# Performance work log

Measured on AMD Instinct MI355X. Metric: run time of the kernel, lower is better.

## Reference

```python
import jax, jax.numpy as jnp
import numpy as np

NEG_SLOPE = 0.1


def setup_inputs() -> dict:
    key = jax.random.key(0)
    k1, k2, k3 = jax.random.split(key, 3)
    l, b, d = 96, 16, 512
    x = jax.random.normal(k1, (l, b, d), dtype=jnp.float32)
    # nn.Linear(2*d, d): weight (d, 2*d), bias (d,)
    W = jax.random.normal(k2, (d, 2 * d), dtype=jnp.float32) * (1.0 / np.sqrt(2 * d))
    bias = jax.random.normal(k3, (d,), dtype=jnp.float32) * 0.01
    return {"x": x, "W": W, "bias": bias}


def reference(x, W, bias):
    """CatLayer forward.
    x: (l, b, c) -> out: (l*l, b, c)
    pair[i, j] = Linear(LeakyReLU(concat(x[i], x[j])))
    """
    l, b, c = x.shape
    # Outer pairwise concat: (l, l, b, 2c); first half is x[i], second half x[j]
    xi = jnp.broadcast_to(x[:, None, :, :], (l, l, b, c))
    xj = jnp.broadcast_to(x[None, :, :, :], (l, l, b, c))
    h = jnp.concatenate([xi, xj], axis=-1)          # (l, l, b, 2c)
    h = jax.nn.leaky_relu(h, negative_slope=NEG_SLOPE)
    out = jnp.einsum('ijbk,ck->ijbc', h, W) + bias  # (l, l, b, c)
    return out.reshape(l * l, b, c)
```

## Files before the change

### kernel.cpp

```cpp
#include <hip/hip_runtime.h>
#include <hip/hip_bf16.h>
#include <stdint.h>


typedef __attribute__((ext_vector_type(8))) short short8;
typedef __attribute__((ext_vector_type(4))) float f32x4;

#define L_DIM 96
#define B_DIM 16
#define C_DIM 512
#define M_DIM 1536
#define K_DIM 512
#define N_DIM 1024

__device__ inline unsigned short f32_to_bf16(float f) {
    union { float f; uint32_t u; } c; c.f = f;
    uint32_t u = c.u;
    uint32_t r = (u + 0x7FFFu + ((u >> 16) & 1u)) >> 16;
    return (unsigned short)r;
}

__global__ __launch_bounds__(256) void prep_a(const float* __restrict__ x,
                                              unsigned short* __restrict__ Abf) {
    int t = blockIdx.x * 256 + threadIdx.x;
    const f32x4* src = (const f32x4*)x + (size_t)t * 2;
    f32x4 v0 = src[0], v1 = src[1];
    short8 o;
    float vals[8] = {v0.x, v0.y, v0.z, v0.w, v1.x, v1.y, v1.z, v1.w};
#pragma unroll
    for (int e = 0; e < 8; ++e) {
        float f = vals[e];
        f = f > 0.f ? f : 0.1f * f;
        o[e] = (short)f32_to_bf16(f);
    }
    *(short8*)(Abf + (size_t)t * 8) = o;
}

__global__ __launch_bounds__(256) void prep_b(const float* __restrict__ W,
                                              unsigned short* __restrict__ Bt) {
    int t = blockIdx.x * 256 + threadIdx.x;
    int n  = t >> 6;
    int kc = (t & 63) << 3;
    const float* src = (n < C_DIM) ? (W + (size_t)n * N_DIM + kc)
                                   : (W + (size_t)(n - C_DIM) * N_DIM + C_DIM + kc);
    const f32x4* s4 = (const f32x4*)src;
    f32x4 v0 = s4[0], v1 = s4[1];
    float vals[8] = {v0.x, v0.y, v0.z, v0.w, v1.x, v1.y, v1.z, v1.w};
    short8 o;
#pragma unroll
    for (int e = 0; e < 8; ++e) o[e] = (short)f32_to_bf16(vals[e]);
    *(short8*)(Bt + (size_t)n * K_DIM + kc) = o;
}

#define LDS_STRIDE 40
__global__ __launch_bounds__(256) void gemm_pq(const unsigned short* __restrict__ A,
                                               const unsigned short* __restrict__ Bt,
                                               const float* __restrict__ bias,
                                               float* __restrict__ C) {
    __shared__ unsigned short As[128 * LDS_STRIDE];
    __shared__ unsigned short Bs[128 * LDS_STRIDE];
    const int bm = blockIdx.x;
    const int bn = blockIdx.y;
    const int tid = threadIdx.x;
    const int lane = tid & 63;
    const int w  = tid >> 6;
    const int wr = w >> 1, wc = w & 1;
    const int l15 = lane & 15, l4 = lane >> 4;

    f32x4 acc[4][4] = {};

    for (int kt = 0; kt < K_DIM / 32; ++kt) {
        __syncthreads();
#pragma unroll
        for (int r = 0; r < 2; ++r) {
            int chunk = tid + 256 * r;
            int row = chunk >> 2;
            int kc  = (chunk & 3) << 3;
            short8 va = *(const short8*)(A  + (size_t)(bm * 128 + row) * K_DIM + kt * 32 + kc);
            *(short8*)(&As[row * LDS_STRIDE + kc]) = va;
            short8 vb = *(const short8*)(Bt + (size_t)(bn * 128 + row) * K_DIM + kt * 32 + kc);
            *(short8*)(&Bs[row * LDS_STRIDE + kc]) = vb;
        }
        __syncthreads();
        short8 a[4], b[4];
#pragma unroll
        for (int m = 0; m < 4; ++m)
            a[m] = *(const short8*)(&As[(wr * 64 + m * 16 + l15) * LDS_STRIDE + l4 * 8]);
#pragma unroll
        for (int n = 0; n < 4; ++n)
            b[n] = *(const short8*)(&Bs[(wc * 64 + n * 16 + l15) * LDS_STRIDE + l4 * 8]);
#pragma unroll
        for (int m = 0; m < 4; ++m)
#pragma unroll
            for (int n = 0; n < 4; ++n)
                acc[m][n] = __builtin_amdgcn_mfma_f32_16x16x32_bf16(a[m], b[n], acc[m][n], 0, 0, 0);
    }

#pragma unroll
    for (int m = 0; m < 4; ++m) {
#pragma unroll
        for (int n = 0; n < 4; ++n) {
            int col = bn * 128 + wc * 64 + n * 16 + l15;
            float bv = (col < C_DIM) ? bias[col] : 0.f;
#pragma unroll
            for (int i = 0; i < 4; ++i) {
                int row = bm * 128 + wr * 64 + m * 16 + l4 * 4 + i;
                C[(size_t)row * N_DIM + col] = acc[m][n][i] + bv;
            }
        }
    }
}

__global__ __launch_bounds__(256) void combine_k(const f32x4* __restrict__ PQ,
                                                 f32x4* __restrict__ out) {
    const uint32_t total = (uint32_t)L_DIM * L_DIM * B_DIM * (C_DIM / 4);
    const uint32_t stride = gridDim.x * blockDim.x;
    for (uint32_t idx = blockIdx.x * blockDim.x + threadIdx.x; idx < total; idx += stride) {
        uint32_t c4 = idx & 127u;
        uint32_t r  = idx >> 7;
        uint32_t b  = r & 15u;
        uint32_t ij = r >> 4;
        uint32_t i  = ij / 96u;
        uint32_t j  = ij - i * 96u;
        f32x4 p = PQ[((size_t)(i * 16u + b)) * 256u + c4];
        f32x4 q = PQ[((size_t)(j * 16u + b)) * 256u + 128u + c4];
        out[idx] = p + q;
    }
}

extern "C" void kernel_launch(void* const* d_in, const int* in_sizes, int n_in,
                              void* d_out, int out_size, void* d_ws, size_t ws_size,
                              hipStream_t stream) {
    const float* x    = (const float*)d_in[0];
    const float* W    = (const float*)d_in[1];
    const float* bias = (const float*)d_in[2];
    float* out = (float*)d_out;

    char* ws = (char*)d_ws;
    unsigned short* Abf = (unsigned short*)ws;
    unsigned short* Bt  = (unsigned short*)(ws + 1572864);
    float*          PQ  = (float*)(ws + 2621440);

    prep_a<<<384, 256, 0, stream>>>(x, Abf);
    prep_b<<<256, 256, 0, stream>>>(W, Bt);
    dim3 g(M_DIM / 128, N_DIM / 128);
    gemm_pq<<<g, 256, 0, stream>>>(Abf, Bt, bias, PQ);
    combine_k<<<4096, 256, 0, stream>>>((const f32x4*)PQ, (f32x4*)out);
}
```

Measured before the change: 79.91 us.

## Fuse bf16 conversion into GEMM loads and restructure combine to reuse P rows

Removes the two prep kernels by loading fp32 x and W directly in the GEMM tile loader and applying LeakyReLU plus bf16 rounding before writing to LDS. This saves two launches and the bf16 staging buffers, at the cost of doubling global load bytes per GEMM tile. The combine kernel is rewritten so each thread holds one P vector in registers and loops over 48 j values with nontemporal stores, which removes the per-element index division and redundant P loads.

```diff
diff --git a/kernel.cpp b/kernel.cpp
--- a/kernel.cpp
+++ b/kernel.cpp
@@ -4,6 +4,7 @@
 
 
 typedef __attribute__((ext_vector_type(8))) short short8;
+typedef __attribute__((ext_vector_type(4))) short short4v;
 typedef __attribute__((ext_vector_type(4))) float f32x4;
 
 #define L_DIM 96
@@ -20,41 +21,9 @@
     return (unsigned short)r;
 }
 
-__global__ __launch_bounds__(256) void prep_a(const float* __restrict__ x,
-                                              unsigned short* __restrict__ Abf) {
-    int t = blockIdx.x * 256 + threadIdx.x;
-    const f32x4* src = (const f32x4*)x + (size_t)t * 2;
-    f32x4 v0 = src[0], v1 = src[1];
-    short8 o;
-    float vals[8] = {v0.x, v0.y, v0.z, v0.w, v1.x, v1.y, v1.z, v1.w};
-#pragma unroll
-    for (int e = 0; e < 8; ++e) {
-        float f = vals[e];
-        f = f > 0.f ? f : 0.1f * f;
-        o[e] = (short)f32_to_bf16(f);
-    }
-    *(short8*)(Abf + (size_t)t * 8) = o;
-}
-
-__global__ __launch_bounds__(256) void prep_b(const float* __restrict__ W,
-                                              unsigned short* __restrict__ Bt) {
-    int t = blockIdx.x * 256 + threadIdx.x;
-    int n  = t >> 6;
-    int kc = (t & 63) << 3;
-    const float* src = (n < C_DIM) ? (W + (size_t)n * N_DIM + kc)
-                                   : (W + (size_t)(n - C_DIM) * N_DIM + C_DIM + kc);
-    const f32x4* s4 = (const f32x4*)src;
-    f32x4 v0 = s4[0], v1 = s4[1];
-    float vals[8] = {v0.x, v0.y, v0.z, v0.w, v1.x, v1.y, v1.z, v1.w};
-    short8 o;
-#pragma unroll
-    for (int e = 0; e < 8; ++e) o[e] = (short)f32_to_bf16(vals[e]);
-    *(short8*)(Bt + (size_t)n * K_DIM + kc) = o;
-}
-
 #define LDS_STRIDE 40
-__global__ __launch_bounds__(256) void gemm_pq(const unsigned short* __restrict__ A,
-                                               const unsigned short* __restrict__ Bt,
+__global__ __launch_bounds__(256) void gemm_pq(const float* __restrict__ x,
+                                               const float* __restrict__ W,
                                                const float* __restrict__ bias,
                                                float* __restrict__ C) {
     __shared__ unsigned short As[128 * LDS_STRIDE];
@@ -67,19 +36,33 @@
     const int wr = w >> 1, wc = w & 1;
     const int l15 = lane & 15, l4 = lane >> 4;
 
+    const float* wbase = (bn < 4) ? (W + (size_t)(bn * 128) * N_DIM)
+                                  : (W + (size_t)(bn * 128 - C_DIM) * N_DIM + C_DIM);
+    const float* xbase = x + (size_t)(bm * 128) * K_DIM;
+
     f32x4 acc[4][4] = {};
 
     for (int kt = 0; kt < K_DIM / 32; ++kt) {
         __syncthreads();
 #pragma unroll
-        for (int r = 0; r < 2; ++r) {
+        for (int r = 0; r < 4; ++r) {
             int chunk = tid + 256 * r;
-            int row = chunk >> 2;
-            int kc  = (chunk & 3) << 3;
-            short8 va = *(const short8*)(A  + (size_t)(bm * 128 + row) * K_DIM + kt * 32 + kc);
-            *(short8*)(&As[row * LDS_STRIDE + kc]) = va;
-            short8 vb = *(const short8*)(Bt + (size_t)(bn * 128 + row) * K_DIM + kt * 32 + kc);
-            *(short8*)(&Bs[row * LDS_STRIDE + kc]) = vb;
+            int row = chunk >> 3;
+            int kc  = (chunk & 7) << 2;
+            f32x4 va = *(const f32x4*)(xbase + (size_t)row * K_DIM + kt * 32 + kc);
+            short4v sa;
+#pragma unroll
+            for (int e = 0; e < 4; ++e) {
+                float f = va[e];
+                f = f > 0.f ? f : 0.1f * f;
+                sa[e] = (short)f32_to_bf16(f);
+            }
+            *(short4v*)(&As[row * LDS_STRIDE + kc]) = sa;
+            f32x4 vb = *(const f32x4*)(wbase + (size_t)row * N_DIM + kt * 32 + kc);
+            short4v sb;
+#pragma unroll
+            for (int e = 0; e < 4; ++e) sb[e] = (short)f32_to_bf16(vb[e]);
+            *(short4v*)(&Bs[row * LDS_STRIDE + kc]) = sb;
         }
         __syncthreads();
         short8 a[4], b[4];
@@ -113,18 +96,23 @@
 
 __global__ __launch_bounds__(256) void combine_k(const f32x4* __restrict__ PQ,
                                                  f32x4* __restrict__ out) {
-    const uint32_t total = (uint32_t)L_DIM * L_DIM * B_DIM * (C_DIM / 4);
-    const uint32_t stride = gridDim.x * blockDim.x;
-    for (uint32_t idx = blockIdx.x * blockDim.x + threadIdx.x; idx < total; idx += stride) {
-        uint32_t c4 = idx & 127u;
-        uint32_t r  = idx >> 7;
-        uint32_t b  = r & 15u;
-        uint32_t ij = r >> 4;
-        uint32_t i  = ij / 96u;
-        uint32_t j  = ij - i * 96u;
-        f32x4 p = PQ[((size_t)(i * 16u + b)) * 256u + c4];
-        f32x4 q = PQ[((size_t)(j * 16u + b)) * 256u + 128u + c4];
-        out[idx] = p + q;
+    const int jh   = blockIdx.x & 1;
+    const int rest = blockIdx.x >> 1;
+    const int t    = rest * 256 + threadIdx.x;
+    const uint32_t c4 = t & 127u;
+    const uint32_t r  = (uint32_t)t >> 7;
+    const uint32_t b  = r & 15u;
+    const uint32_t i  = r >> 4;
+
+    const f32x4 p = PQ[(size_t)r * 256u + c4];
+    const f32x4* qrow = PQ + (size_t)b * 256u + 128u + c4;
+    f32x4* orow = out + ((size_t)(i * 96u) * 16u + b) * 128u + c4;
+
+    const int j0 = jh * 48, j1 = j0 + 48;
+#pragma unroll 4
+    for (int j = j0; j < j1; ++j) {
+        f32x4 q = qrow[(size_t)j * 16u * 256u];
+        __builtin_nontemporal_store(p + q, orow + (size_t)j * 16u * 128u);
     }
 }
 
@@ -136,14 +124,9 @@
     const float* bias = (const float*)d_in[2];
     float* out = (float*)d_out;
 
-    char* ws = (char*)d_ws;
-    unsigned short* Abf = (unsigned short*)ws;
-    unsigned short* Bt  = (unsigned short*)(ws + 1572864);
-    float*          PQ  = (float*)(ws + 2621440);
+    float* PQ = (float*)d_ws;
 
-    prep_a<<<384, 256, 0, stream>>>(x, Abf);
-    prep_b<<<256, 256, 0, stream>>>(W, Bt);
     dim3 g(M_DIM / 128, N_DIM / 128);
-    gemm_pq<<<g, 256, 0, stream>>>(Abf, Bt, bias, PQ);
-    combine_k<<<4096, 256, 0, stream>>>((const f32x4*)PQ, (f32x4*)out);
+    gemm_pq<<<g, 256, 0, stream>>>(x, W, bias, PQ);
+    combine_k<<<1536, 256, 0, stream>>>((const f32x4*)PQ, (f32x4*)out);
 }
```

After: 77.88 us. 2.5% less time.
